# Optimization experiments

Measured on AMD Instinct MI355X. Metric: run time of the kernel, lower is better.

Reference implementation:

```python
import jax, jax.numpy as jnp
import numpy as np


def setup_inputs() -> dict:
    key = jax.random.key(0)
    k1, k2, k3 = jax.random.split(key, 3)
    B, N, M, C = 4, 4096, 8192, 64
    PPU = 64.0  # points_per_unit
    xz = jax.random.normal(k1, (B, M, 1), dtype=jnp.float32) * 10.0  # grid locations
    z = jax.random.normal(k2, (B, C, M), dtype=jnp.float32)          # channels-first features
    x = jax.random.normal(k3, (B, N, 1), dtype=jnp.float32) * 10.0   # query locations
    log_scale = jnp.asarray(np.log(2.0 / PPU), dtype=jnp.float32)
    return {"xz": xz, "z": z, "x": x, "log_scale": log_scale}


def reference(xz, z, x, log_scale):
    # pairwise squared distances between x [B,N,1] and xz [B,M,1] -> [B,N,M]
    diff = x - jnp.swapaxes(xz, -1, -2)            # [B,N,M]
    dists2 = diff * diff
    # RBF weights (no normalization)
    weights = jnp.exp(-0.5 * dists2 / jnp.exp(2.0 * log_scale))  # [B,N,M]
    # z: [B,C,M] -> transpose -> [B,M,C]; weights @ z^T -> [B,N,C]
    out = jnp.einsum('bnm,bcm->bnc', weights, z)
    return out
```

## Files before the change

kernel.cpp:

```cpp
#include <hip/hip_runtime.h>
#include <math.h>

#define B 4
#define N 4096
#define M 8192
#define C 64
#define NB 2048
#define XMIN (-64.0f)
#define INV_BW 16.0f
#define CUT 8.0f
#define QG 16
#define PCH 64

__device__ __forceinline__ int bucket_of(float v) {
    int k = (int)floorf((v - XMIN) * INV_BW);
    return min(max(k, 0), NB - 1);
}

__global__ __launch_bounds__(1024) void bin_kernel(
    const float* __restrict__ xz, const float* __restrict__ x,
    int* __restrict__ bucket_start,
    float* __restrict__ xs,
    int* __restrict__ islot,
    float* __restrict__ qcs,
    int* __restrict__ qis)
{
    const int t    = threadIdx.x;
    const int lane = t & 63;
    const int w    = t >> 6;

    __shared__ int hist[NB];
    __shared__ int run[NB];
    __shared__ int wsum[16];
    const bool isQ = blockIdx.x >= 4;
    const int  b   = blockIdx.x & 3;
    const int  PT  = isQ ? (N / 1024) : (M / 1024);
    const float* src = isQ ? (x + b * N) : (xz + b * M);

    hist[t] = 0; hist[t + 1024] = 0;
    __syncthreads();

    float pv[8]; int pk[8];
    for (int j = 0; j < PT; ++j) {
        float v = src[j * 1024 + t];
        pv[j] = v; pk[j] = bucket_of(v);
        atomicAdd(&hist[pk[j]], 1);
    }
    __syncthreads();

    const int h0 = hist[2 * t], h1 = hist[2 * t + 1];
    const int tot = h0 + h1;
    int s = tot;
    #pragma unroll
    for (int off = 1; off < 64; off <<= 1) {
        int up = __shfl_up(s, off, 64);
        if (lane >= off) s += up;
    }
    if (lane == 63) wsum[w] = s;
    __syncthreads();
    int woff = 0;
    for (int i = 0; i < w; ++i) woff += wsum[i];
    const int excl = woff + s - tot;

    run[2 * t]     = excl;
    run[2 * t + 1] = excl + h0;
    if (!isQ) {
        bucket_start[b * (NB + 1) + 2 * t]     = excl;
        bucket_start[b * (NB + 1) + 2 * t + 1] = excl + h0;
        if (t == 1023) bucket_start[b * (NB + 1) + NB] = woff + s;
    }
    __syncthreads();

    if (!isQ) {
        for (int j = 0; j < PT; ++j) {
            int slot = atomicAdd(&run[pk[j]], 1);
            xs[b * M + slot]           = pv[j];
            islot[b * M + j * 1024 + t] = slot;
        }
    } else {
        for (int j = 0; j < PT; ++j) {
            int slot = atomicAdd(&run[pk[j]], 1);
            qcs[b * N + slot] = pv[j];
            qis[b * N + slot] = j * 1024 + t;
        }
    }
}

__global__ __launch_bounds__(1024) void permz_kernel(
    const float* __restrict__ z, const int* __restrict__ islot,
    float* __restrict__ zs)
{
    const int t  = threadIdx.x;
    const int b  = blockIdx.x >> 7;
    const int m0 = (blockIdx.x & 127) * 64;
    __shared__ float tile[64][65];
    __shared__ int slot_s[64];

    const int m = t & 63;
    #pragma unroll
    for (int k = 0; k < 4; ++k) {
        int c = (t >> 6) + 16 * k;
        tile[c][m] = z[((size_t)b * C + c) * M + m0 + m];
    }
    if (t < 64) slot_s[t] = islot[b * M + m0 + t];
    __syncthreads();

    const int j  = t >> 4;
    const int c4 = t & 15;
    float4 v4 = make_float4(tile[c4 * 4 + 0][j], tile[c4 * 4 + 1][j],
                            tile[c4 * 4 + 2][j], tile[c4 * 4 + 3][j]);
    ((float4*)zs)[((size_t)b * M + slot_s[j]) * 16 + c4] = v4;
}

__global__ __launch_bounds__(256) void gather_kernel(
    const float* __restrict__ log_scale,
    const int* __restrict__ bucket_start,
    const float* __restrict__ xs,
    const float* __restrict__ qcs,
    const int* __restrict__ qis,
    const float* __restrict__ zs,
    float* __restrict__ out)
{
    const int t    = threadIdx.x;
    const int lane = t & 63;
    const int w    = t >> 6;
    const int g  = blockIdx.x;
    const int b  = g >> 8;
    const int g0 = (g & 255) * QG;

    __shared__ __align__(16) float zr[PCH][C];
    __shared__ __align__(16) float wl[QG][PCH];
    __shared__ float qc[QG];
    __shared__ int   qi[QG];

    const float ls   = log_scale[0];
    const float coef = -0.5f * __expf(-2.0f * ls);
    const float R    = sqrtf(CUT / (-coef));

    if (t < QG) {
        qc[t] = qcs[b * N + g0 + t];
        qi[t] = qis[b * N + g0 + t];
    }
    __syncthreads();

    float xmin = qc[0], xmax = qc[0];
    #pragma unroll
    for (int j = 1; j < QG; ++j) {
        xmin = fminf(xmin, qc[j]);
        xmax = fmaxf(xmax, qc[j]);
    }
    const int s0 = bucket_start[b * (NB + 1) + bucket_of(xmin - R)];
    const int s1 = bucket_start[b * (NB + 1) + bucket_of(xmax + R) + 1];

    const float q0 = qc[w * 4 + 0], q1 = qc[w * 4 + 1];
    const float q2 = qc[w * 4 + 2], q3 = qc[w * 4 + 3];

    if (s0 >= s1) {
        out[((size_t)b * N + qi[w * 4 + 0]) * C + lane] = 0.0f;
        out[((size_t)b * N + qi[w * 4 + 1]) * C + lane] = 0.0f;
        out[((size_t)b * N + qi[w * 4 + 2]) * C + lane] = 0.0f;
        out[((size_t)b * N + qi[w * 4 + 3]) * C + lane] = 0.0f;
        return;
    }

    float a0 = 0.f, a1 = 0.f, a2 = 0.f, a3 = 0.f;

    const float*  xsb = xs + b * M;
    const float4* zs4 = (const float4*)zs + (size_t)b * M * 16;

    for (int cs = s0; cs < s1; cs += PCH) {
        const int cnt = min(PCH, s1 - cs);
        __syncthreads();
        #pragma unroll
        for (int r = 0; r < 4; ++r) {
            const float4* gp = zs4 + ((size_t)cs) * 16 + r * 256 + w * 64 + lane;
            float* lp = &zr[r * 16 + w * 4][0];
            __builtin_amdgcn_global_load_lds(
                (const __attribute__((address_space(1))) void*)gp,
                (__attribute__((address_space(3))) void*)lp, 16, 0, 0);
        }
        {
            const float pcr   = xsb[cs + lane];
            const bool  valid = (cs + lane) < s1;
            float d0 = q0 - pcr, d1 = q1 - pcr, d2 = q2 - pcr, d3 = q3 - pcr;
            wl[w * 4 + 0][lane] = valid ? __expf(coef * d0 * d0) : 0.0f;
            wl[w * 4 + 1][lane] = valid ? __expf(coef * d1 * d1) : 0.0f;
            wl[w * 4 + 2][lane] = valid ? __expf(coef * d2 * d2) : 0.0f;
            wl[w * 4 + 3][lane] = valid ? __expf(coef * d3 * d3) : 0.0f;
        }
        __syncthreads();
        for (int p = 0; p < cnt; p += 4) {
            float zv0 = zr[p + 0][lane];
            float zv1 = zr[p + 1][lane];
            float zv2 = zr[p + 2][lane];
            float zv3 = zr[p + 3][lane];
            const float4 wa = *(const float4*)&wl[w * 4 + 0][p];
            const float4 wb = *(const float4*)&wl[w * 4 + 1][p];
            const float4 wc = *(const float4*)&wl[w * 4 + 2][p];
            const float4 wd = *(const float4*)&wl[w * 4 + 3][p];
            a0 = fmaf(wa.x, zv0, a0); a0 = fmaf(wa.y, zv1, a0);
            a0 = fmaf(wa.z, zv2, a0); a0 = fmaf(wa.w, zv3, a0);
            a1 = fmaf(wb.x, zv0, a1); a1 = fmaf(wb.y, zv1, a1);
            a1 = fmaf(wb.z, zv2, a1); a1 = fmaf(wb.w, zv3, a1);
            a2 = fmaf(wc.x, zv0, a2); a2 = fmaf(wc.y, zv1, a2);
            a2 = fmaf(wc.z, zv2, a2); a2 = fmaf(wc.w, zv3, a2);
            a3 = fmaf(wd.x, zv0, a3); a3 = fmaf(wd.y, zv1, a3);
            a3 = fmaf(wd.z, zv2, a3); a3 = fmaf(wd.w, zv3, a3);
        }
    }

    out[((size_t)b * N + qi[w * 4 + 0]) * C + lane] = a0;
    out[((size_t)b * N + qi[w * 4 + 1]) * C + lane] = a1;
    out[((size_t)b * N + qi[w * 4 + 2]) * C + lane] = a2;
    out[((size_t)b * N + qi[w * 4 + 3]) * C + lane] = a3;
}

extern "C" void kernel_launch(void* const* d_in, const int* in_sizes, int n_in,
                              void* d_out, int out_size, void* d_ws, size_t ws_size,
                              hipStream_t stream) {
    const float* xz = (const float*)d_in[0];
    const float* z  = (const float*)d_in[1];
    const float* x  = (const float*)d_in[2];
    const float* ls = (const float*)d_in[3];
    float* out = (float*)d_out;

    char* ws = (char*)d_ws;
    size_t off = 0;
    auto alloc = [&](size_t bytes) { void* p = ws + off; off += (bytes + 255) & ~size_t(255); return p; };

    float* zs    = (float*)alloc(((size_t)B * M + 64) * C * sizeof(float));
    float* xs    = (float*)alloc(((size_t)B * M + 64) * sizeof(float));
    int*   islot = (int*)alloc((size_t)B * M * sizeof(int));
    float* qcs   = (float*)alloc((size_t)B * N * sizeof(float));
    int*   qis   = (int*)alloc((size_t)B * N * sizeof(int));
    int*   bst   = (int*)alloc((size_t)B * (NB + 1) * sizeof(int));

    bin_kernel<<<8, 1024, 0, stream>>>(xz, x, bst, xs, islot, qcs, qis);
    permz_kernel<<<512, 1024, 0, stream>>>(z, islot, zs);
    gather_kernel<<<B * (N / QG), 256, 0, stream>>>(ls, bst, xs, qcs, qis, zs, out);
}
```

Before: 92.32 us.

## Use bf16 MFMA for RBF-weighted gather with bf16 permuted features

The permuted feature table is now stored as bf16 instead of fp32, and the per-chunk weighted accumulation is replaced by 16x16x32 bf16 MFMA instructions. Each wave computes its weight fragments directly in registers, so the shared-memory weight buffer goes away. The distance cutoff is widened to offset the precision change. This targets the scalar FMA loop and halves gather bandwidth, at the cost of bf16 rounding of both weights and features, and strided 2-byte LDS reads when building the B fragments.

```diff
diff --git a/kernel.cpp b/kernel.cpp
--- a/kernel.cpp
+++ b/kernel.cpp
@@ -8,13 +8,20 @@
 #define NB 2048
 #define XMIN (-64.0f)
 #define INV_BW 16.0f
-#define CUT 8.0f
+#define CUT 10.0f
 #define QG 16
-#define PCH 64
+
+typedef __attribute__((ext_vector_type(8))) short short8;
+typedef __attribute__((ext_vector_type(4))) float f32x4;
 
 __device__ __forceinline__ int bucket_of(float v) {
     int k = (int)floorf((v - XMIN) * INV_BW);
     return min(max(k, 0), NB - 1);
+}
+
+__device__ __forceinline__ unsigned short f2bf(float f) {
+    unsigned int u = __float_as_uint(f);
+    return (unsigned short)((u + 0x7FFF + ((u >> 16) & 1)) >> 16);
 }
 
 __global__ __launch_bounds__(1024) void bin_kernel(
@@ -74,7 +81,7 @@
     if (!isQ) {
         for (int j = 0; j < PT; ++j) {
             int slot = atomicAdd(&run[pk[j]], 1);
-            xs[b * M + slot]           = pv[j];
+            xs[b * M + slot]            = pv[j];
             islot[b * M + j * 1024 + t] = slot;
         }
     } else {
@@ -88,7 +95,7 @@
 
 __global__ __launch_bounds__(1024) void permz_kernel(
     const float* __restrict__ z, const int* __restrict__ islot,
-    float* __restrict__ zs)
+    unsigned short* __restrict__ zs)
 {
     const int t  = threadIdx.x;
     const int b  = blockIdx.x >> 7;
@@ -107,9 +114,12 @@
 
     const int j  = t >> 4;
     const int c4 = t & 15;
-    float4 v4 = make_float4(tile[c4 * 4 + 0][j], tile[c4 * 4 + 1][j],
-                            tile[c4 * 4 + 2][j], tile[c4 * 4 + 3][j]);
-    ((float4*)zs)[((size_t)b * M + slot_s[j]) * 16 + c4] = v4;
+    ushort4 v4;
+    v4.x = f2bf(tile[c4 * 4 + 0][j]);
+    v4.y = f2bf(tile[c4 * 4 + 1][j]);
+    v4.z = f2bf(tile[c4 * 4 + 2][j]);
+    v4.w = f2bf(tile[c4 * 4 + 3][j]);
+    ((ushort4*)zs)[((size_t)b * M + slot_s[j]) * 16 + c4] = v4;
 }
 
 __global__ __launch_bounds__(256) void gather_kernel(
@@ -118,101 +128,89 @@
     const float* __restrict__ xs,
     const float* __restrict__ qcs,
     const int* __restrict__ qis,
-    const float* __restrict__ zs,
+    const unsigned short* __restrict__ zs,
     float* __restrict__ out)
 {
     const int t    = threadIdx.x;
     const int lane = t & 63;
     const int w    = t >> 6;
+    const int quad = lane >> 4;
+    const int low4 = lane & 15;
     const int g  = blockIdx.x;
     const int b  = g >> 8;
     const int g0 = (g & 255) * QG;
 
-    __shared__ __align__(16) float zr[PCH][C];
-    __shared__ __align__(16) float wl[QG][PCH];
-    __shared__ float qc[QG];
-    __shared__ int   qi[QG];
+    __shared__ unsigned short zr[64 * 64];
+    __shared__ float qcS[QG];
+    __shared__ int   qiS[QG];
 
     const float ls   = log_scale[0];
     const float coef = -0.5f * __expf(-2.0f * ls);
     const float R    = sqrtf(CUT / (-coef));
 
     if (t < QG) {
-        qc[t] = qcs[b * N + g0 + t];
-        qi[t] = qis[b * N + g0 + t];
-    }
-    __syncthreads();
-
-    float xmin = qc[0], xmax = qc[0];
+        qcS[t] = qcs[b * N + g0 + t];
+        qiS[t] = qis[b * N + g0 + t];
+    }
+    __syncthreads();
+
+    float xmin = qcS[0], xmax = qcS[0];
     #pragma unroll
     for (int j = 1; j < QG; ++j) {
-        xmin = fminf(xmin, qc[j]);
-        xmax = fmaxf(xmax, qc[j]);
+        xmin = fminf(xmin, qcS[j]);
+        xmax = fmaxf(xmax, qcS[j]);
     }
     const int s0 = bucket_start[b * (NB + 1) + bucket_of(xmin - R)];
     const int s1 = bucket_start[b * (NB + 1) + bucket_of(xmax + R) + 1];
 
-    const float q0 = qc[w * 4 + 0], q1 = qc[w * 4 + 1];
-    const float q2 = qc[w * 4 + 2], q3 = qc[w * 4 + 3];
-
-    if (s0 >= s1) {
-        out[((size_t)b * N + qi[w * 4 + 0]) * C + lane] = 0.0f;
-        out[((size_t)b * N + qi[w * 4 + 1]) * C + lane] = 0.0f;
-        out[((size_t)b * N + qi[w * 4 + 2]) * C + lane] = 0.0f;
-        out[((size_t)b * N + qi[w * 4 + 3]) * C + lane] = 0.0f;
-        return;
-    }
-
-    float a0 = 0.f, a1 = 0.f, a2 = 0.f, a3 = 0.f;
-
-    const float*  xsb = xs + b * M;
-    const float4* zs4 = (const float4*)zs + (size_t)b * M * 16;
-
-    for (int cs = s0; cs < s1; cs += PCH) {
-        const int cnt = min(PCH, s1 - cs);
+    const float qv = qcS[low4];
+    f32x4 acc = {0.f, 0.f, 0.f, 0.f};
+
+    const float* xsb = xs + b * M;
+    const unsigned short* zsb = zs + (size_t)b * M * C;
+
+    for (int cs = s0; cs < s1; cs += 64) {
         __syncthreads();
         #pragma unroll
-        for (int r = 0; r < 4; ++r) {
-            const float4* gp = zs4 + ((size_t)cs) * 16 + r * 256 + w * 64 + lane;
-            float* lp = &zr[r * 16 + w * 4][0];
+        for (int r = 0; r < 2; ++r) {
+            const unsigned short* gp =
+                zsb + ((size_t)cs + (w * 2 + r) * 8 + (lane >> 3)) * C + (lane & 7) * 8;
+            unsigned short* lp = zr + (w * 2 + r) * 512;
             __builtin_amdgcn_global_load_lds(
                 (const __attribute__((address_space(1))) void*)gp,
                 (__attribute__((address_space(3))) void*)lp, 16, 0, 0);
         }
-        {
-            const float pcr   = xsb[cs + lane];
-            const bool  valid = (cs + lane) < s1;
-            float d0 = q0 - pcr, d1 = q1 - pcr, d2 = q2 - pcr, d3 = q3 - pcr;
-            wl[w * 4 + 0][lane] = valid ? __expf(coef * d0 * d0) : 0.0f;
-            wl[w * 4 + 1][lane] = valid ? __expf(coef * d1 * d1) : 0.0f;
-            wl[w * 4 + 2][lane] = valid ? __expf(coef * d2 * d2) : 0.0f;
-            wl[w * 4 + 3][lane] = valid ? __expf(coef * d3 * d3) : 0.0f;
+        short8 afrag[2];
+        #pragma unroll
+        for (int kh = 0; kh < 2; ++kh) {
+            #pragma unroll
+            for (int j = 0; j < 8; ++j) {
+                const int k = kh * 32 + quad * 8 + j;
+                const float xp = xsb[cs + k];
+                const float d  = qv - xp;
+                float wgt = __expf(coef * d * d);
+                wgt = (cs + k < s1) ? wgt : 0.0f;
+                afrag[kh][j] = (short)f2bf(wgt);
+            }
         }
         __syncthreads();
-        for (int p = 0; p < cnt; p += 4) {
-            float zv0 = zr[p + 0][lane];
-            float zv1 = zr[p + 1][lane];
-            float zv2 = zr[p + 2][lane];
-            float zv3 = zr[p + 3][lane];
-            const float4 wa = *(const float4*)&wl[w * 4 + 0][p];
-            const float4 wb = *(const float4*)&wl[w * 4 + 1][p];
-            const float4 wc = *(const float4*)&wl[w * 4 + 2][p];
-            const float4 wd = *(const float4*)&wl[w * 4 + 3][p];
-            a0 = fmaf(wa.x, zv0, a0); a0 = fmaf(wa.y, zv1, a0);
-            a0 = fmaf(wa.z, zv2, a0); a0 = fmaf(wa.w, zv3, a0);
-            a1 = fmaf(wb.x, zv0, a1); a1 = fmaf(wb.y, zv1, a1);
-            a1 = fmaf(wb.z, zv2, a1); a1 = fmaf(wb.w, zv3, a1);
-            a2 = fmaf(wc.x, zv0, a2); a2 = fmaf(wc.y, zv1, a2);
-            a2 = fmaf(wc.z, zv2, a2); a2 = fmaf(wc.w, zv3, a2);
-            a3 = fmaf(wd.x, zv0, a3); a3 = fmaf(wd.y, zv1, a3);
-            a3 = fmaf(wd.z, zv2, a3); a3 = fmaf(wd.w, zv3, a3);
-        }
-    }
-
-    out[((size_t)b * N + qi[w * 4 + 0]) * C + lane] = a0;
-    out[((size_t)b * N + qi[w * 4 + 1]) * C + lane] = a1;
-    out[((size_t)b * N + qi[w * 4 + 2]) * C + lane] = a2;
-    out[((size_t)b * N + qi[w * 4 + 3]) * C + lane] = a3;
+        #pragma unroll
+        for (int kh = 0; kh < 2; ++kh) {
+            short8 bfrag;
+            #pragma unroll
+            for (int j = 0; j < 8; ++j) {
+                const int p = kh * 32 + quad * 8 + j;
+                bfrag[j] = (short)zr[p * 64 + w * 16 + low4];
+            }
+            acc = __builtin_amdgcn_mfma_f32_16x16x32_bf16(afrag[kh], bfrag, acc, 0, 0, 0);
+        }
+    }
+
+    #pragma unroll
+    for (int r = 0; r < 4; ++r) {
+        const int q = quad * 4 + r;
+        out[((size_t)b * N + qiS[q]) * C + w * 16 + low4] = acc[r];
+    }
 }
 
 extern "C" void kernel_launch(void* const* d_in, const int* in_sizes, int n_in,
@@ -228,7 +226,7 @@
     size_t off = 0;
     auto alloc = [&](size_t bytes) { void* p = ws + off; off += (bytes + 255) & ~size_t(255); return p; };
 
-    float* zs    = (float*)alloc(((size_t)B * M + 64) * C * sizeof(float));
+    unsigned short* zs = (unsigned short*)alloc(((size_t)B * M + 64) * C * sizeof(unsigned short));
     float* xs    = (float*)alloc(((size_t)B * M + 64) * sizeof(float));
     int*   islot = (int*)alloc((size_t)B * M * sizeof(int));
     float* qcs   = (float*)alloc((size_t)B * N * sizeof(float));
```

Result: faster. 89.42 us (-3.1%).
